# Kernel optimization log

Measured on AMD Instinct MI355X. Metric: run time of the kernel, lower is better.

Reference implementation:

```python
import jax, jax.numpy as jnp
import numpy as np

STRIDE = 16
PRE_K = 600
POST_K = 100
NMS_T = 0.7


def _gen_anchors(base=16.0, ratios=(0.5, 1.0, 2.0), scales=(8.0, 16.0, 32.0)):
    a = []
    for s in scales:
        for r in ratios:
            w = base * s * (r ** 0.5)
            h = base * s / (r ** 0.5)
            a.append([-w / 2, -h / 2, w / 2, h / 2])
    return jnp.asarray(a, jnp.float32)  # [9,4]


def _conv(x, w, b, pad):
    y = jax.lax.conv_general_dilated(x, w, (1, 1), [(pad, pad), (pad, pad)],
                                     dimension_numbers=("NCHW", "OIHW", "NCHW"))
    return y + b[None, :, None, None]


def _decode(deltas, anchors):
    w = anchors[:, 2] - anchors[:, 0]
    h = anchors[:, 3] - anchors[:, 1]
    cx = anchors[:, 0] + 0.5 * w
    cy = anchors[:, 1] + 0.5 * h
    dx, dy, dw, dh = deltas[:, 0], deltas[:, 1], deltas[:, 2], deltas[:, 3]
    pcx = cx + dx * w
    pcy = cy + dy * h
    pw = w * jnp.exp(dw)
    ph = h * jnp.exp(dh)
    return jnp.stack([pcx - 0.5 * pw, pcy - 0.5 * ph,
                      pcx + 0.5 * pw, pcy + 0.5 * ph], axis=-1)


def _nms_keep(boxes, thresh):
    # boxes already sorted by score descending; returns bool keep mask [N]
    x1, y1, x2, y2 = boxes[:, 0], boxes[:, 1], boxes[:, 2], boxes[:, 3]
    area = (x2 - x1) * (y2 - y1)
    xx1 = jnp.maximum(x1[:, None], x1[None, :])
    yy1 = jnp.maximum(y1[:, None], y1[None, :])
    xx2 = jnp.minimum(x2[:, None], x2[None, :])
    yy2 = jnp.minimum(y2[:, None], y2[None, :])
    inter = jnp.maximum(xx2 - xx1, 0.0) * jnp.maximum(yy2 - yy1, 0.0)
    iou = inter / (area[:, None] + area[None, :] - inter)
    n = boxes.shape[0]
    idx = jnp.arange(n)

    def body(i, keep):
        suppress = keep[i] & (iou[i] > thresh) & (idx > i)
        return keep & ~suppress

    return jax.lax.fori_loop(0, n, body, jnp.ones((n,), bool))


def setup_inputs() -> dict:
    key = jax.random.key(0)
    ks = jax.random.split(key, 7)
    C_in, C_mid, A = 256, 256, 9
    feats = jax.random.normal(ks[0], (4, C_in, 128, 128), jnp.float32)
    conv_w = jax.random.normal(ks[1], (C_mid, C_in, 3, 3), jnp.float32) * 0.02
    conv_b = jnp.zeros((C_mid,), jnp.float32)
    cls_w = jax.random.normal(ks[2], (A, C_mid, 1, 1), jnp.float32) * 0.05
    cls_b = jnp.zeros((A,), jnp.float32)
    bbox_w = jax.random.normal(ks[3], (A * 4, C_mid, 1, 1), jnp.float32) * 0.02
    bbox_b = jnp.zeros((A * 4,), jnp.float32)
    return {"features": feats, "conv_w": conv_w, "conv_b": conv_b,
            "cls_w": cls_w, "cls_b": cls_b, "bbox_w": bbox_w, "bbox_b": bbox_b,
            "image_h": 2048, "image_w": 2048}


def reference(features, conv_w, conv_b, cls_w, cls_b, bbox_w, bbox_b, image_h, image_w):
    B, _, H, W = features.shape
    A = cls_w.shape[0]
    t = jax.nn.relu(_conv(features, conv_w, conv_b, 1))
    logits = _conv(t, cls_w, cls_b, 0)        # [B,A,H,W]
    bbox_deltas = _conv(t, bbox_w, bbox_b, 0)  # [B,4A,H,W]

    anchors = _gen_anchors()
    sx = jnp.arange(W, dtype=jnp.float32) * STRIDE
    sy = jnp.arange(H, dtype=jnp.float32) * STRIDE
    gy, gx = jnp.meshgrid(sy, sx, indexing="ij")
    shifts = jnp.stack([gx, gy, gx, gy], axis=2).reshape(-1, 4)  # [HW,4]
    anchors_all = (anchors[None, :, :] + shifts[:, None, :]).reshape(-1, 4)  # [HW*A,4]

    scores = jnp.transpose(logits, (0, 2, 3, 1)).reshape(B, -1)          # [B,HWA]
    deltas = jnp.transpose(bbox_deltas, (0, 2, 3, 1)).reshape(B, -1, 4)  # [B,HWA,4]

    img_w = jnp.float32(image_w)
    img_h = jnp.float32(image_h)

    def per_image(s, d):
        p = _decode(d, anchors_all)
        p = jnp.stack([jnp.clip(p[:, 0], 0.0, img_w),
                       jnp.clip(p[:, 1], 0.0, img_h),
                       jnp.clip(p[:, 2], 0.0, img_w),
                       jnp.clip(p[:, 3], 0.0, img_h)], axis=-1)
        _, topi = jax.lax.top_k(s, PRE_K)
        p = p[topi]                                # [PRE_K,4] sorted by score
        keep = _nms_keep(p, NMS_T)
        order = jnp.argsort(jnp.where(keep, 0, 1), stable=True)  # kept first, score order
        sel = order[:POST_K]
        valid = keep[sel]
        return p[sel] * valid[:, None].astype(p.dtype)  # zero-pad suppressed slots

    return jax.vmap(per_image)(scores, deltas)  # [B,POST_K,4]
```

## Files before the change

kernel.cpp:

```cpp
#include <hip/hip_runtime.h>
#include <cstdint>
#include <cstddef>

#define BB 4
#define CIN 256
#define HH 128
#define WW 128
#define NANCH (HH*WW*9)
#define PRE_K 600
#define POST_K 100
#define NMS_T 0.7f
#define CAND_CAP 2048

typedef _Float16 f16x8 __attribute__((ext_vector_type(8)));
typedef float    f32x4 __attribute__((ext_vector_type(4)));

#define WS_SCORES 0
#define WS_DELTAS (BB*NANCH)
#define WS_WHI    (WS_DELTAS + BB*NANCH*4)
#define WS_WLO    (WS_WHI + 9*256*128)
#define WS_HIST   (WS_WLO + 9*256*128)
#define WS_CCNT   (WS_HIST + 8192)
#define WS_CAND   (WS_CCNT + 16)
#define WS_PHI    (WS_CAND + 16384)
#define WS_PLANE_F 8388608
#define WS_PLO    (WS_PHI + WS_PLANE_F)
#define WS_ZERO   (WS_PLO + WS_PLANE_F)
#define WS_TOTAL_FULL (WS_ZERO + 16)
#define WS_TOTAL_MIN  WS_PHI

__device__ inline unsigned score_key(float f) {
    unsigned u = __float_as_uint(f);
    return (u & 0x80000000u) ? ~u : (u | 0x80000000u);
}

__global__ __launch_bounds__(256)
void prep_all(const float* __restrict__ feat, const float* __restrict__ convw,
              _Float16* __restrict__ pHi, _Float16* __restrict__ pLo,
              _Float16* __restrict__ whi, _Float16* __restrict__ wlo,
              float* __restrict__ zeroPg, unsigned* __restrict__ ghist,
              int prepBlocks)
{
    const int blk = blockIdx.x;
    if (blk < prepBlocks) {
        const int id = blk * 256 + threadIdx.x;
        if (blk == 0 && threadIdx.x < 16) zeroPg[threadIdx.x] = 0.f;
        const int gx = id & 127;
        const int gy = (id >> 7) & 127;
        const int ck = (id >> 14) & 7;
        const int b  = id >> 17;
        const int g  = (((gx + 1) >> 1) & 1) | (((gy + 1) & 1) << 1);
        const float* fb = feat + ((size_t)(b*256 + ck*32) << 14) + (gy << 7) + gx;
        f16x8 gh[4], gl[4];
        #pragma unroll
        for (int icg = 0; icg < 4; ++icg)
            #pragma unroll
            for (int k = 0; k < 8; ++k) {
                const float v = fb[(size_t)(icg*8 + k) << 14] * 16.f;
                const _Float16 h = (_Float16)v;
                gh[icg][k] = h;
                gl[icg][k] = (_Float16)(v - (float)h);
            }
        char* Hc = (char*)pHi + (size_t)id * 64;
        char* Lc = (char*)pLo + (size_t)id * 64;
        #pragma unroll
        for (int icg = 0; icg < 4; ++icg) {
            const int p = icg ^ g;
            *(f16x8*)(Hc + p*16) = gh[icg];
            *(f16x8*)(Lc + p*16) = gl[icg];
        }
    } else if (blk < prepBlocks + 256) {
        const int g = (blk - prepBlocks) * 256 + threadIdx.x;
        if (g >= 65536) return;
        const int oc = g >> 8, ic = g & 255;
        const int chunk = ic >> 5, icl = ic & 31;
        #pragma unroll
        for (int t = 0; t < 9; ++t) {
            const float v = convw[(size_t)g*9 + t] * 64.f;
            const _Float16 h = (_Float16)v;
            const _Float16 lo = (_Float16)(v - (float)h);
            const size_t o = (size_t)((t*8 + chunk)*256 + oc)*32 + icl;
            whi[o] = h;
            wlo[o] = lo;
        }
    } else {
        const int id = (blk - prepBlocks - 256) * 256 + threadIdx.x;
        if (id < 8208) ghist[id] = 0u;
    }
}

__global__ __launch_bounds__(512, 2)
void conv_mfma(const float* __restrict__ feat, const float* __restrict__ convb,
               const _Float16* __restrict__ whi, const _Float16* __restrict__ wlo,
               const float* __restrict__ clsw, const float* __restrict__ bboxw,
               const float* __restrict__ clsb, const float* __restrict__ bboxb,
               const _Float16* __restrict__ pHi, const _Float16* __restrict__ pLo,
               const float* __restrict__ zeroPg, unsigned* __restrict__ ghist,
               float* __restrict__ scores, float* __restrict__ deltas)
{
    __shared__ __align__(16) unsigned char smem[87040];
    float* sBias = (float*)(smem + 86016);

    const int bid = blockIdx.x;
    const int b  = bid >> 6;
    const int ty = (bid >> 3) & 7;
    const int tx = bid & 7;
    const int h0 = ty*16, c0 = tx*16;
    const int tid = threadIdx.x;
    const int w   = tid >> 6;
    const int wm  = w >> 1;
    const int wph = w & 1;
    const int l  = tid & 63;
    const int q  = l >> 4;
    const int c  = l & 15;

    const float* featb = feat + (size_t)b*CIN*HH*WW;
    const int wOff = (wm*64 + c)*32 + q*8;

    if (tid < 256) sBias[tid] = convb[tid] * 1024.f;

    int sdesc[3];
    #pragma unroll
    for (int it = 0; it < 3; ++it) {
        const int e = it*512 + tid;
        if (e < 1344) {
            const int Yl = e / 72, rem = e - Yl*72;
            const int Xl = rem >> 2, p = rem & 3;
            const int gy = h0 - 1 + Yl, gx = c0 - 1 + Xl;
            sdesc[it] = (((unsigned)gy < 128u) && ((unsigned)gx < 128u))
                        ? ((((gy << 7) + gx) << 6) + (p << 4)) : -1;
        } else sdesc[it] = -2;
    }

    auto stage = [&](int ck, int buf) {
        unsigned char* hb = smem + buf*21504;
        unsigned char* lb = smem + 43008 + buf*21504;
        if (pHi) {
            const size_t pb = ((size_t)(b*8 + ck)) << 20;
            #pragma unroll
            for (int pl = 0; pl < 2; ++pl) {
                const char* Ps = (const char*)(pl ? pLo : pHi) + pb;
                unsigned char* Pd = pl ? lb : hb;
                #pragma unroll
                for (int it = 0; it < 3; ++it) {
                    if (sdesc[it] != -2) {
                        const char* src = (sdesc[it] >= 0) ? Ps + sdesc[it]
                                                           : (const char*)zeroPg;
                        __builtin_amdgcn_global_load_lds(
                            (const __attribute__((address_space(1))) void*)src,
                            (__attribute__((address_space(3))) void*)(Pd + it*8192 + tid*16),
                            16, 0, 0);
                    }
                }
            }
        } else {
            const int ic0s = ck*32;
            for (int e = tid; e < 1296; e += 512) {
                const int icg = e / 324, s = e - icg*324;
                const int Y = s / 18, X = s - Y*18;
                const int gy = h0 - 1 + Y, gx = c0 - 1 + X;
                const int g = ((X >> 1) & 1) | ((Y & 1) << 1);
                const bool inb = ((unsigned)gy < 128u) && ((unsigned)gx < 128u);
                f16x8 hv, lv;
                #pragma unroll
                for (int k = 0; k < 8; ++k) {
                    float v = 0.f;
                    if (inb) v = featb[((size_t)(ic0s + icg*8 + k)*HH + gy)*WW + gx];
                    v *= 16.f;
                    const _Float16 h = (_Float16)v;
                    hv[k] = h;
                    lv[k] = (_Float16)(v - (float)h);
                }
                const int base = s*64 + ((icg ^ g) << 4);
                *(f16x8*)(hb + base) = hv;
                *(f16x8*)(lb + base) = lv;
            }
        }
    };

    stage(0, 0);
    __syncthreads();

    f32x4 acc[4][8];
    #pragma unroll
    for (int mf = 0; mf < 4; ++mf) {
        const f32x4 bv = *(const f32x4*)(sBias + (wm*64 + mf*16 + 4*q));
        #pragma unroll
        for (int nf = 0; nf < 8; ++nf) acc[mf][nf] = bv;
    }

    for (int chunk = 0; chunk < 8; ++chunk) {
        const int cur = chunk & 1;
        if (chunk + 1 < 8) stage(chunk + 1, cur ^ 1);
        const unsigned char* hb = smem + cur*21504;
        const unsigned char* lb = smem + 43008 + cur*21504;

        #pragma unroll 3
        for (int t = 0; t < 9; ++t) {
            const int ky = t / 3, kx = t - ky*3;
            const _Float16* pWh = whi + (size_t)(t*8 + chunk)*8192 + wOff;
            const _Float16* pWl = wlo + (size_t)(t*8 + chunk)*8192 + wOff;
            f16x8 ah[4], al[4];
            #pragma unroll
            for (int mf = 0; mf < 4; ++mf) {
                ah[mf] = *(const f16x8*)(const void*)(pWh + mf*512);
                al[mf] = *(const f16x8*)(const void*)(pWl + mf*512);
            }
            #pragma unroll
            for (int nfh = 0; nfh < 2; ++nfh) {
                f16x8 bh[4], bl[4];
                #pragma unroll
                for (int j = 0; j < 4; ++j) {
                    const int nf = nfh*4 + j;
                    const int Y = wph*8 + (nf >> 1)*2 + (c >> 3) + ky;
                    const int X = (nf & 1)*8 + (c & 7) + kx;
                    const int g = ((X >> 1) & 1) | ((Y & 1) << 1);
                    const int addr = (Y*18 + X)*64 + ((q ^ g) << 4);
                    bh[j] = *(const f16x8*)(hb + addr);
                    bl[j] = *(const f16x8*)(lb + addr);
                }
                #pragma unroll
                for (int mf = 0; mf < 4; ++mf)
                    #pragma unroll
                    for (int j = 0; j < 4; ++j) {
                        acc[mf][nfh*4+j] = __builtin_amdgcn_mfma_f32_16x16x32_f16(ah[mf], bh[j], acc[mf][nfh*4+j], 0, 0, 0);
                        acc[mf][nfh*4+j] = __builtin_amdgcn_mfma_f32_16x16x32_f16(ah[mf], bl[j], acc[mf][nfh*4+j], 0, 0, 0);
                        acc[mf][nfh*4+j] = __builtin_amdgcn_mfma_f32_16x16x32_f16(al[mf], bh[j], acc[mf][nfh*4+j], 0, 0, 0);
                    }
            }
        }
        __syncthreads();
    }

    #pragma unroll
    for (int mf = 0; mf < 4; ++mf)
        #pragma unroll
        for (int nf = 0; nf < 8; ++nf)
            #pragma unroll
            for (int r = 0; r < 4; ++r)
                acc[mf][nf][r] = fmaxf(acc[mf][nf][r], 0.f) * 0.0009765625f;

    float*    sW15  = (float*)smem;
    float*    sPart = (float*)(smem + 15360);
    unsigned* sHist = (unsigned*)(smem + 76800);

    for (int e = tid; e < 2048; e += 512) sHist[e] = 0u;

    for (int g = 0; g < 3; ++g) {
        __syncthreads();
        for (int e = tid; e < 3840; e += 512) {
            const int chl = e >> 8, o = e & 255;
            const int ch = g*15 + chl;
            sW15[e] = (ch < 9) ? clsw[ch*256 + o] : bboxw[(ch - 9)*256 + o];
        }
        __syncthreads();
        for (int chl = 0; chl < 15; ++chl) {
            f32x4 wv[4];
            #pragma unroll
            for (int mf = 0; mf < 4; ++mf)
                wv[mf] = *(const f32x4*)(sW15 + chl*256 + wm*64 + mf*16 + 4*q);
            float p[8];
            #pragma unroll
            for (int nf = 0; nf < 8; ++nf) {
                float s = 0.f;
                #pragma unroll
                for (int mf = 0; mf < 4; ++mf)
                    #pragma unroll
                    for (int r = 0; r < 4; ++r)
                        s += wv[mf][r] * acc[mf][nf][r];
                s += __shfl_xor(s, 16, 64);
                s += __shfl_xor(s, 32, 64);
                p[nf] = s;
            }
            const float v0 = (q == 0) ? p[0] : (q == 1) ? p[1] : (q == 2) ? p[2] : p[3];
            const float v1 = (q == 0) ? p[4] : (q == 1) ? p[5] : (q == 2) ? p[6] : p[7];
            sPart[(w*15 + chl)*128 + q*16 + c]      = v0;
            sPart[(w*15 + chl)*128 + 64 + q*16 + c] = v1;
        }
        __syncthreads();
        for (int e = tid; e < 3840; e += 512) {
            const int chl = e >> 8, pxg = e & 255;
            const int ph = pxg >> 7, pxl = pxg & 127;
            float s = 0.f;
            #pragma unroll
            for (int wmq = 0; wmq < 4; ++wmq)
                s += sPart[((wmq*2 + ph)*15 + chl)*128 + pxl];
            const int ch = g*15 + chl;
            s += (ch < 9) ? clsb[ch] : bboxb[ch - 9];
            const int nf = pxl >> 4, cc2 = pxl & 15;
            const int Y = ph*8 + (nf >> 1)*2 + (cc2 >> 3);
            const int X = (nf & 1)*8 + (cc2 & 7);
            const int gy = h0 + Y, gx = c0 + X;
            const int n4 = gy*WW + gx;
            if (ch < 9) {
                scores[(size_t)b*NANCH + n4*9 + ch] = s;
                atomicAdd(&sHist[score_key(s) >> 21], 1u);
            } else {
                const int cc = ch - 9;
                deltas[((size_t)b*NANCH + n4*9 + (cc >> 2))*4 + (cc & 3)] = s;
            }
        }
    }
    for (int e = tid; e < 2048; e += 512) {
        const unsigned cv = sHist[e];
        if (cv) atomicAdd(&ghist[b*2048 + e], cv);
    }
}

__device__ inline void find_thresh(const unsigned* hist, int NB, unsigned target, unsigned* shv)
{
    const int tid = threadIdx.x;
    if (tid < 64) {
        const int gsz = NB >> 5;
        unsigned gsum = 0;
        if (tid < 32)
            for (int k = 0; k < gsz; ++k)
                gsum += hist[tid*gsz + ((k + tid) & (gsz-1))];
        unsigned suf = gsum;
        #pragma unroll
        for (int d = 1; d < 32; d <<= 1) {
            const unsigned t = __shfl_down(suf, d, 64);
            if (tid + d < 32) suf += t;
        }
        const unsigned long long m = __ballot(tid < 32 && suf >= target);
        const int G = 63 - __clzll(m);
        unsigned caboveG = 0;
        { const unsigned t = __shfl(suf, G+1, 64); if (G < 31) caboveG = t; }
        unsigned h = 0;
        if (tid < gsz) h = hist[G*gsz + tid];
        unsigned wsuf = h;
        #pragma unroll
        for (int d = 1; d < 64; d <<= 1) {
            const unsigned t = __shfl_down(wsuf, d, 64);
            if (tid + d < gsz) wsuf += t;
        }
        const unsigned long long m2 = __ballot(tid < gsz && (caboveG + wsuf) >= target);
        const int L = 63 - __clzll(m2);
        if (tid == L) { shv[0] = (unsigned)(G*gsz + L); shv[1] = caboveG + wsuf - h; }
    }
}

__global__ __launch_bounds__(256)
void filter_kernel(const float* __restrict__ scores, const unsigned* __restrict__ ghist,
                   unsigned* __restrict__ ccnt, unsigned long long* __restrict__ cand)
{
    __shared__ unsigned h[2048];
    __shared__ unsigned shv[8];
    const int blk = blockIdx.x;
    const int b = blk >> 6, s = blk & 63;
    const int tid = threadIdx.x;
    const unsigned* hb = ghist + b*2048;
    for (int e = tid; e < 2048; e += 256) h[e] = hb[e];
    __syncthreads();
    find_thresh(h, 2048, PRE_K, shv);
    __syncthreads();
    const unsigned T1 = shv[0];
    const unsigned C  = shv[1] + h[T1];
    const float* si = scores + (size_t)b*NANCH + s*2304;
    if (C <= (unsigned)CAND_CAP) {
        #pragma unroll
        for (int k = 0; k < 9; ++k) {
            const int i = tid + k*256;
            const unsigned u = score_key(si[i]);
            if ((u >> 21) >= T1) {
                const unsigned p = atomicAdd(&ccnt[b], 1u);
                cand[(size_t)b*CAND_CAP + p] =
                    ((unsigned long long)(~u) << 32) | (unsigned)(s*2304 + i);
            }
        }
    } else if (s == 0 && tid == 0) {
        ccnt[b] = 0x7FFFFFFFu;
    }
}

__device__ inline unsigned long long shfl_u64(unsigned long long v, int src) {
    const int lo = __shfl((int)(v & 0xffffffffull), src, 64);
    const int hi = __shfl((int)(v >> 32), src, 64);
    return ((unsigned long long)(unsigned)hi << 32) | (unsigned)lo;
}

__global__ __launch_bounds__(1024)
void post_kernel(const float* __restrict__ scores, const float* __restrict__ deltas,
                 const unsigned* __restrict__ ccnt, const unsigned long long* __restrict__ cand,
                 const int* __restrict__ imh, const int* __restrict__ imw,
                 float* __restrict__ out)
{
    __shared__ unsigned hist[2048];
    __shared__ unsigned long long arr[1024];
    __shared__ unsigned tiebuf[1024];
    __shared__ unsigned shv[8];
    __shared__ unsigned long long arr2[CAND_CAP];
    __shared__ float bx[PRE_K][4];
    __shared__ unsigned long long mrow[PRE_K][10];
    __shared__ unsigned long long keepw[10];
    __shared__ unsigned wpfx[11];
    __shared__ int sel[POST_K];
    const int b = blockIdx.x, tid = threadIdx.x;
    const float* si = scores + (size_t)b*NANCH;

    const unsigned n = ccnt[b];
    const bool fast = (n <= (unsigned)CAND_CAP);
    if (fast) {
        for (int e = tid; e < CAND_CAP; e += 1024)
            arr2[e] = (e < (int)n) ? cand[(size_t)b*CAND_CAP + e] : ~0ull;
        for (unsigned k = 2; k <= (unsigned)CAND_CAP; k <<= 1)
            for (unsigned j = k >> 1; j > 0; j >>= 1) {
                __syncthreads();
                #pragma unroll
                for (int hh = 0; hh < 2; ++hh) {
                    const unsigned i = (unsigned)tid + hh*1024, ixj = i ^ j;
                    if (ixj > i) {
                        const unsigned long long a = arr2[i], c2 = arr2[ixj];
                        if ((a > c2) == ((i & k) == 0)) { arr2[i] = c2; arr2[ixj] = a; }
                    }
                }
            }
        __syncthreads();
    } else {
        for (int i = tid; i < 2048; i += 1024) hist[i] = 0;
        __syncthreads();
        for (int i = tid; i < NANCH; i += 1024)
            atomicAdd(&hist[score_key(si[i]) >> 21], 1u);
        __syncthreads();
        find_thresh(hist, 2048, PRE_K, shv);
        __syncthreads();
        const unsigned T1 = shv[0], gtA = shv[1];
        __syncthreads();

        for (int i = tid; i < 2048; i += 1024) hist[i] = 0;
        __syncthreads();
        for (int i = tid; i < NANCH; i += 1024) {
            const unsigned u = score_key(si[i]);
            if ((u >> 21) == T1) atomicAdd(&hist[(u >> 10) & 0x7FFu], 1u);
        }
        __syncthreads();
        find_thresh(hist, 2048, PRE_K - gtA, shv);
        __syncthreads();
        const unsigned T2 = shv[0], gtB = shv[1];
        const unsigned top22 = (T1 << 11) | T2;
        __syncthreads();

        for (int i = tid; i < 1024; i += 1024) hist[i] = 0;
        __syncthreads();
        for (int i = tid; i < NANCH; i += 1024) {
            const unsigned u = score_key(si[i]);
            if ((u >> 10) == top22) atomicAdd(&hist[u & 0x3FFu], 1u);
        }
        __syncthreads();
        find_thresh(hist, 1024, PRE_K - gtA - gtB, shv);
        if (tid == 0) { shv[4] = 0; shv[5] = 0; }
        __syncthreads();
        const unsigned u_thr = (top22 << 10) | shv[0];
        const unsigned n_greater = gtA + gtB + shv[1];
        __syncthreads();

        for (int i = tid; i < NANCH; i += 1024) {
            const unsigned u = score_key(si[i]);
            if (u > u_thr) {
                const unsigned p = atomicAdd(&shv[4], 1u);
                arr[p] = ((unsigned long long)(~u) << 32) | (unsigned)i;
            } else if (u == u_thr) {
                const unsigned p = atomicAdd(&shv[5], 1u);
                if (p < 1024u) tiebuf[p] = (unsigned)i;
            }
        }
        __syncthreads();
        const unsigned cnt_tie = (shv[5] > 1024u) ? 1024u : shv[5];
        if ((unsigned)tid >= cnt_tie) tiebuf[tid] = 0xFFFFFFFFu;

        for (unsigned k = 2; k <= 1024; k <<= 1)
            for (unsigned j = k >> 1; j > 0; j >>= 1) {
                __syncthreads();
                const unsigned i = (unsigned)tid, ixj = i ^ j;
                if (ixj > i) {
                    const unsigned a = tiebuf[i], cc = tiebuf[ixj];
                    if ((a > cc) == ((i & k) == 0)) { tiebuf[i] = cc; tiebuf[ixj] = a; }
                }
            }
        __syncthreads();
        const unsigned ties_needed = PRE_K - n_greater;
        if ((unsigned)tid < ties_needed)
            arr[n_greater + tid] = ((unsigned long long)(~u_thr) << 32) | tiebuf[tid];
        if (tid >= PRE_K) arr[tid] = ~0ull;

        for (unsigned k = 2; k <= 1024; k <<= 1)
            for (unsigned j = k >> 1; j > 0; j >>= 1) {
                __syncthreads();
                const unsigned i = (unsigned)tid, ixj = i ^ j;
                if (ixj > i) {
                    const unsigned long long a = arr[i], cc = arr[ixj];
                    if ((a > cc) == ((i & k) == 0)) { arr[i] = cc; arr[ixj] = a; }
                }
            }
        __syncthreads();
        if (tid < 1024) arr2[tid] = arr[tid];
        __syncthreads();
    }

    if (tid < PRE_K) {
        const unsigned idx = (unsigned)arr2[tid];
        const int a   = (int)(idx % 9u);
        const int n4  = (int)(idx / 9u);
        const int hh_ = n4 >> 7;
        const int ww_ = n4 & 127;
        const int si_ = a / 3, ri = a % 3;
        const double sq = (ri == 0) ? 0.70710678118654752440 : ((ri == 1) ? 1.0 : 1.41421356237309504880);
        const double sc = (si_ == 0) ? 8.0 : ((si_ == 1) ? 16.0 : 32.0);
        const float half_w = (float)(16.0 * sc * sq * 0.5);
        const float half_h = (float)(16.0 * sc / sq * 0.5);
        const float shx = 16.f * (float)ww_;
        const float shy = 16.f * (float)hh_;
        const float x1a = shx - half_w, x2a = shx + half_w;
        const float y1a = shy - half_h, y2a = shy + half_h;
        const float aw = x2a - x1a, ah = y2a - y1a;
        const float acx = x1a + 0.5f*aw, acy = y1a + 0.5f*ah;
        const float* d = deltas + ((size_t)b*NANCH + idx) * 4;
        const float dx = d[0], dy = d[1], dw = d[2], dh = d[3];
        const float pcx = acx + dx*aw;
        const float pcy = acy + dy*ah;
        const float pw  = aw * expf(dw);
        const float ph  = ah * expf(dh);
        const float fw = (float)imw[0], fh = (float)imh[0];
        bx[tid][0] = fminf(fmaxf(pcx - 0.5f*pw, 0.f), fw);
        bx[tid][1] = fminf(fmaxf(pcy - 0.5f*ph, 0.f), fh);
        bx[tid][2] = fminf(fmaxf(pcx + 0.5f*pw, 0.f), fw);
        bx[tid][3] = fminf(fmaxf(pcy + 0.5f*ph, 0.f), fh);
    }
    __syncthreads();

    for (int item = tid; item < PRE_K*10; item += 1024) {
        const int i  = item / 10;
        const int wj = item - i*10;
        unsigned long long m = 0ull;
        const int jbase = wj * 64;
        if (jbase + 63 > i) {
            const float xi1 = bx[i][0], yi1 = bx[i][1], xi2 = bx[i][2], yi2 = bx[i][3];
            const float ai = (xi2 - xi1) * (yi2 - yi1);
            for (int bit = 0; bit < 64; ++bit) {
                const int j = jbase + bit;
                if (j < PRE_K && j > i) {
                    const float xx1 = fmaxf(xi1, bx[j][0]);
                    const float yy1 = fmaxf(yi1, bx[j][1]);
                    const float xx2 = fminf(xi2, bx[j][2]);
                    const float yy2 = fminf(yi2, bx[j][3]);
                    const float inter = fmaxf(xx2 - xx1, 0.f) * fmaxf(yy2 - yy1, 0.f);
                    const float aj = (bx[j][2] - bx[j][0]) * (bx[j][3] - bx[j][1]);
                    const float iou = inter / (ai + aj - inter);
                    if (iou > NMS_T) m |= (1ull << bit);
                }
            }
        }
        mrow[i][wj] = m;
    }
    __syncthreads();

    if (tid < 64) {
        const int lane = tid;
        unsigned long long kwv;
        if (lane < 9)       kwv = ~0ull;
        else if (lane == 9) kwv = (1ull << (PRE_K - 576)) - 1;
        else                kwv = 0ull;
        for (int w = 0; w < 10; ++w) {
            const int base = w*64;
            const int nb = (w == 9) ? (PRE_K - 576) : 64;
            if (lane == w) {
                for (int bit = 0; bit < nb; ++bit) {
                    const unsigned long long mm = mrow[base + bit][w];
                    if ((kwv >> bit) & 1ull) kwv &= ~mm;
                }
            }
            const unsigned long long fw = shfl_u64(kwv, w);
            if (lane > w && lane < 10) {
                for (int bit = 0; bit < nb; ++bit) {
                    const unsigned long long mm = mrow[base + bit][lane];
                    if ((fw >> bit) & 1ull) kwv &= ~mm;
                }
            }
        }
        if (lane < 10) keepw[lane] = kwv;
    }
    __syncthreads();
    if (tid == 0) {
        unsigned ccount = 0;
        #pragma unroll
        for (int w = 0; w < 10; ++w) { wpfx[w] = ccount; ccount += (unsigned)__popcll(keepw[w]); }
        wpfx[10] = ccount;
    }
    if (tid < POST_K) sel[tid] = -1;
    __syncthreads();
    if (tid < PRE_K) {
        const int w = tid >> 6, bit = tid & 63;
        const unsigned long long kw = keepw[w];
        if ((kw >> bit) & 1ull) {
            const unsigned rank = wpfx[w] + (unsigned)__popcll(kw & ((1ull << bit) - 1ull));
            if (rank < POST_K) sel[rank] = tid;
        }
    }
    __syncthreads();
    if (tid < POST_K) {
        const int s_ = sel[tid];
        float o0 = 0.f, o1 = 0.f, o2 = 0.f, o3 = 0.f;
        if (s_ >= 0) { o0 = bx[s_][0]; o1 = bx[s_][1]; o2 = bx[s_][2]; o3 = bx[s_][3]; }
        float* o = out + (size_t)b*POST_K*4 + tid*4;
        o[0] = o0; o[1] = o1; o[2] = o2; o[3] = o3;
    }
}

extern "C" void kernel_launch(void* const* d_in, const int* in_sizes, int n_in,
                              void* d_out, int out_size, void* d_ws, size_t ws_size,
                              hipStream_t stream) {
    const float* feat  = (const float*)d_in[0];
    const float* convw = (const float*)d_in[1];
    const float* convb = (const float*)d_in[2];
    const float* clsw  = (const float*)d_in[3];
    const float* clsb  = (const float*)d_in[4];
    const float* bboxw = (const float*)d_in[5];
    const float* bboxb = (const float*)d_in[6];
    const int*   imh   = (const int*)d_in[7];
    const int*   imw   = (const int*)d_in[8];

    if (ws_size < (size_t)WS_TOTAL_MIN * sizeof(float)) return;
    const bool use_prep = ws_size >= (size_t)WS_TOTAL_FULL * sizeof(float);

    float*    scores = (float*)d_ws + WS_SCORES;
    float*    deltas = (float*)d_ws + WS_DELTAS;
    _Float16* whi    = (_Float16*)((float*)d_ws + WS_WHI);
    _Float16* wlo    = (_Float16*)((float*)d_ws + WS_WLO);
    unsigned* ghist  = (unsigned*)((float*)d_ws + WS_HIST);
    unsigned* ccnt   = (unsigned*)((float*)d_ws + WS_CCNT);
    unsigned long long* cand = (unsigned long long*)((float*)d_ws + WS_CAND);
    _Float16* pHi    = use_prep ? (_Float16*)((float*)d_ws + WS_PHI) : nullptr;
    _Float16* pLo    = use_prep ? (_Float16*)((float*)d_ws + WS_PLO) : nullptr;
    float*    zeroPg = use_prep ? ((float*)d_ws + WS_ZERO) : nullptr;
    float*    outp   = (float*)d_out;

    const int prepBlocks = use_prep ? 2048 : 0;
    prep_all<<<dim3(prepBlocks + 256 + 33), dim3(256), 0, stream>>>(
        feat, convw, pHi, pLo, whi, wlo, zeroPg, ghist, prepBlocks);
    conv_mfma<<<dim3(256), dim3(512), 0, stream>>>(feat, convb, whi, wlo, clsw, bboxw,
                                                   clsb, bboxb, pHi, pLo, zeroPg, ghist,
                                                   scores, deltas);
    filter_kernel<<<dim3(256), dim3(256), 0, stream>>>(scores, ghist, ccnt, cand);
    post_kernel<<<dim3(BB), dim3(1024), 0, stream>>>(scores, deltas, ccnt, cand,
                                                     imh, imw, outp);
}
```

Baseline: 440.2 us.

## Replace candidate bitonic sort with radix-select top-K and precompute conv LDS addresses

Result: slower. 532.2 us (+20.9%).

```diff
diff --git a/kernel.cpp b/kernel.cpp
--- a/kernel.cpp
+++ b/kernel.cpp
@@ -10,7 +10,7 @@
 #define PRE_K 600
 #define POST_K 100
 #define NMS_T 0.7f
-#define CAND_CAP 2048
+#define CAND_CAP 8192
 
 typedef _Float16 f16x8 __attribute__((ext_vector_type(8)));
 typedef float    f32x4 __attribute__((ext_vector_type(4)));
@@ -22,7 +22,7 @@
 #define WS_HIST   (WS_WLO + 9*256*128)
 #define WS_CCNT   (WS_HIST + 8192)
 #define WS_CAND   (WS_CCNT + 16)
-#define WS_PHI    (WS_CAND + 16384)
+#define WS_PHI    (WS_CAND + BB*CAND_CAP*2)
 #define WS_PLANE_F 8388608
 #define WS_PLO    (WS_PHI + WS_PLANE_F)
 #define WS_ZERO   (WS_PLO + WS_PLANE_F)
@@ -118,6 +118,23 @@
     const int wOff = (wm*64 + c)*32 + q*8;
 
     if (tid < 256) sBias[tid] = convb[tid] * 1024.f;
+
+    int rcbase[8];
+    #pragma unroll
+    for (int nf = 0; nf < 8; ++nf) {
+        const int by = wph*8 + (nf >> 1)*2 + (c >> 3);
+        const int bxx = (nf & 1)*8 + (c & 7);
+        rcbase[nf] = (by*18 + bxx)*64;
+    }
+    int xort[3][2];
+    #pragma unroll
+    for (int kx = 0; kx < 3; ++kx)
+        #pragma unroll
+        for (int kyp = 0; kyp < 2; ++kyp) {
+            const int gxb = (((c & 7) + kx) >> 1) & 1;
+            const int gyb = (((c >> 3) + kyp) & 1) << 1;
+            xort[kx][kyp] = ((q ^ (gxb | gyb)) << 4);
+        }
 
     int sdesc[3];
     #pragma unroll
@@ -195,9 +212,10 @@
         const unsigned char* hb = smem + cur*21504;
         const unsigned char* lb = smem + 43008 + cur*21504;
 
-        #pragma unroll 3
+        #pragma unroll
         for (int t = 0; t < 9; ++t) {
             const int ky = t / 3, kx = t - ky*3;
+            const int tconst = (ky*18 + kx)*64;
             const _Float16* pWh = whi + (size_t)(t*8 + chunk)*8192 + wOff;
             const _Float16* pWl = wlo + (size_t)(t*8 + chunk)*8192 + wOff;
             f16x8 ah[4], al[4];
@@ -212,10 +230,7 @@
                 #pragma unroll
                 for (int j = 0; j < 4; ++j) {
                     const int nf = nfh*4 + j;
-                    const int Y = wph*8 + (nf >> 1)*2 + (c >> 3) + ky;
-                    const int X = (nf & 1)*8 + (c & 7) + kx;
-                    const int g = ((X >> 1) & 1) | ((Y & 1) << 1);
-                    const int addr = (Y*18 + X)*64 + ((q ^ g) << 4);
+                    const int addr = rcbase[nf] + tconst + xort[kx][ky & 1];
                     bh[j] = *(const f16x8*)(hb + addr);
                     bl[j] = *(const f16x8*)(lb + addr);
                 }
@@ -385,11 +400,11 @@
                  const int* __restrict__ imh, const int* __restrict__ imw,
                  float* __restrict__ out)
 {
+    __shared__ unsigned long long cnd[CAND_CAP];
     __shared__ unsigned hist[2048];
     __shared__ unsigned long long arr[1024];
     __shared__ unsigned tiebuf[1024];
     __shared__ unsigned shv[8];
-    __shared__ unsigned long long arr2[CAND_CAP];
     __shared__ float bx[PRE_K][4];
     __shared__ unsigned long long mrow[PRE_K][10];
     __shared__ unsigned long long keepw[10];
@@ -400,60 +415,84 @@
 
     const unsigned n = ccnt[b];
     const bool fast = (n <= (unsigned)CAND_CAP);
+
     if (fast) {
         for (int e = tid; e < CAND_CAP; e += 1024)
-            arr2[e] = (e < (int)n) ? cand[(size_t)b*CAND_CAP + e] : ~0ull;
-        for (unsigned k = 2; k <= (unsigned)CAND_CAP; k <<= 1)
-            for (unsigned j = k >> 1; j > 0; j >>= 1) {
-                __syncthreads();
-                #pragma unroll
-                for (int hh = 0; hh < 2; ++hh) {
-                    const unsigned i = (unsigned)tid + hh*1024, ixj = i ^ j;
-                    if (ixj > i) {
-                        const unsigned long long a = arr2[i], c2 = arr2[ixj];
-                        if ((a > c2) == ((i & k) == 0)) { arr2[i] = c2; arr2[ixj] = a; }
-                    }
-                }
-            }
-        __syncthreads();
+            cnd[e] = (e < (int)n) ? cand[(size_t)b*CAND_CAP + e] : ~0ull;
+    }
+    __syncthreads();
+
+    for (int i = tid; i < 2048; i += 1024) hist[i] = 0;
+    __syncthreads();
+    if (fast) {
+        for (int e = tid; e < (int)n; e += 1024) {
+            const unsigned u = ~(unsigned)(cnd[e] >> 32);
+            atomicAdd(&hist[u >> 21], 1u);
+        }
     } else {
-        for (int i = tid; i < 2048; i += 1024) hist[i] = 0;
-        __syncthreads();
         for (int i = tid; i < NANCH; i += 1024)
             atomicAdd(&hist[score_key(si[i]) >> 21], 1u);
-        __syncthreads();
-        find_thresh(hist, 2048, PRE_K, shv);
-        __syncthreads();
-        const unsigned T1 = shv[0], gtA = shv[1];
-        __syncthreads();
-
-        for (int i = tid; i < 2048; i += 1024) hist[i] = 0;
-        __syncthreads();
+    }
+    __syncthreads();
+    find_thresh(hist, 2048, PRE_K, shv);
+    __syncthreads();
+    const unsigned T1 = shv[0], gtA = shv[1];
+    __syncthreads();
+
+    for (int i = tid; i < 2048; i += 1024) hist[i] = 0;
+    __syncthreads();
+    if (fast) {
+        for (int e = tid; e < (int)n; e += 1024) {
+            const unsigned u = ~(unsigned)(cnd[e] >> 32);
+            if ((u >> 21) == T1) atomicAdd(&hist[(u >> 10) & 0x7FFu], 1u);
+        }
+    } else {
         for (int i = tid; i < NANCH; i += 1024) {
             const unsigned u = score_key(si[i]);
             if ((u >> 21) == T1) atomicAdd(&hist[(u >> 10) & 0x7FFu], 1u);
         }
-        __syncthreads();
-        find_thresh(hist, 2048, PRE_K - gtA, shv);
-        __syncthreads();
-        const unsigned T2 = shv[0], gtB = shv[1];
-        const unsigned top22 = (T1 << 11) | T2;
-        __syncthreads();
-
-        for (int i = tid; i < 1024; i += 1024) hist[i] = 0;
-        __syncthreads();
+    }
+    __syncthreads();
+    find_thresh(hist, 2048, PRE_K - gtA, shv);
+    __syncthreads();
+    const unsigned T2 = shv[0], gtB = shv[1];
+    const unsigned top22 = (T1 << 11) | T2;
+    __syncthreads();
+
+    for (int i = tid; i < 1024; i += 1024) hist[i] = 0;
+    __syncthreads();
+    if (fast) {
+        for (int e = tid; e < (int)n; e += 1024) {
+            const unsigned u = ~(unsigned)(cnd[e] >> 32);
+            if ((u >> 10) == top22) atomicAdd(&hist[u & 0x3FFu], 1u);
+        }
+    } else {
         for (int i = tid; i < NANCH; i += 1024) {
             const unsigned u = score_key(si[i]);
             if ((u >> 10) == top22) atomicAdd(&hist[u & 0x3FFu], 1u);
         }
-        __syncthreads();
-        find_thresh(hist, 1024, PRE_K - gtA - gtB, shv);
-        if (tid == 0) { shv[4] = 0; shv[5] = 0; }
-        __syncthreads();
-        const unsigned u_thr = (top22 << 10) | shv[0];
-        const unsigned n_greater = gtA + gtB + shv[1];
-        __syncthreads();
-
+    }
+    __syncthreads();
+    find_thresh(hist, 1024, PRE_K - gtA - gtB, shv);
+    if (tid == 0) { shv[4] = 0; shv[5] = 0; }
+    __syncthreads();
+    const unsigned u_thr = (top22 << 10) | shv[0];
+    const unsigned n_greater = gtA + gtB + shv[1];
+    __syncthreads();
+
+    if (fast) {
+        for (int e = tid; e < (int)n; e += 1024) {
+            const unsigned long long cv = cnd[e];
+            const unsigned u = ~(unsigned)(cv >> 32);
+            if (u > u_thr) {
+                const unsigned p = atomicAdd(&shv[4], 1u);
+                arr[p] = cv;
+            } else if (u == u_thr) {
+                const unsigned p = atomicAdd(&shv[5], 1u);
+                if (p < 1024u) tiebuf[p] = (unsigned)cv;
+            }
+        }
+    } else {
         for (int i = tid; i < NANCH; i += 1024) {
             const unsigned u = score_key(si[i]);
             if (u > u_thr) {
@@ -464,41 +503,39 @@
                 if (p < 1024u) tiebuf[p] = (unsigned)i;
             }
         }
-        __syncthreads();
-        const unsigned cnt_tie = (shv[5] > 1024u) ? 1024u : shv[5];
-        if ((unsigned)tid >= cnt_tie) tiebuf[tid] = 0xFFFFFFFFu;
-
-        for (unsigned k = 2; k <= 1024; k <<= 1)
-            for (unsigned j = k >> 1; j > 0; j >>= 1) {
-                __syncthreads();
-                const unsigned i = (unsigned)tid, ixj = i ^ j;
-                if (ixj > i) {
-                    const unsigned a = tiebuf[i], cc = tiebuf[ixj];
-                    if ((a > cc) == ((i & k) == 0)) { tiebuf[i] = cc; tiebuf[ixj] = a; }
-                }
-            }
-        __syncthreads();
-        const unsigned ties_needed = PRE_K - n_greater;
-        if ((unsigned)tid < ties_needed)
-            arr[n_greater + tid] = ((unsigned long long)(~u_thr) << 32) | tiebuf[tid];
-        if (tid >= PRE_K) arr[tid] = ~0ull;
-
-        for (unsigned k = 2; k <= 1024; k <<= 1)
-            for (unsigned j = k >> 1; j > 0; j >>= 1) {
-                __syncthreads();
-                const unsigned i = (unsigned)tid, ixj = i ^ j;
-                if (ixj > i) {
-                    const unsigned long long a = arr[i], cc = arr[ixj];
-                    if ((a > cc) == ((i & k) == 0)) { arr[i] = cc; arr[ixj] = a; }
-                }
-            }
-        __syncthreads();
-        if (tid < 1024) arr2[tid] = arr[tid];
-        __syncthreads();
-    }
+    }
+    __syncthreads();
+    const unsigned cnt_tie = (shv[5] > 1024u) ? 1024u : shv[5];
+    if ((unsigned)tid >= cnt_tie) tiebuf[tid] = 0xFFFFFFFFu;
+
+    for (unsigned k = 2; k <= 1024; k <<= 1)
+        for (unsigned j = k >> 1; j > 0; j >>= 1) {
+            __syncthreads();
+            const unsigned i = (unsigned)tid, ixj = i ^ j;
+            if (ixj > i) {
+                const unsigned a = tiebuf[i], cc = tiebuf[ixj];
+                if ((a > cc) == ((i & k) == 0)) { tiebuf[i] = cc; tiebuf[ixj] = a; }
+            }
+        }
+    __syncthreads();
+    const unsigned ties_needed = PRE_K - n_greater;
+    if ((unsigned)tid < ties_needed)
+        arr[n_greater + tid] = ((unsigned long long)(~u_thr) << 32) | tiebuf[tid];
+    if (tid >= PRE_K) arr[tid] = ~0ull;
+
+    for (unsigned k = 2; k <= 1024; k <<= 1)
+        for (unsigned j = k >> 1; j > 0; j >>= 1) {
+            __syncthreads();
+            const unsigned i = (unsigned)tid, ixj = i ^ j;
+            if (ixj > i) {
+                const unsigned long long a = arr[i], cc = arr[ixj];
+                if ((a > cc) == ((i & k) == 0)) { arr[i] = cc; arr[ixj] = a; }
+            }
+        }
+    __syncthreads();
 
     if (tid < PRE_K) {
-        const unsigned idx = (unsigned)arr2[tid];
+        const unsigned idx = (unsigned)arr[tid];
         const int a   = (int)(idx % 9u);
         const int n4  = (int)(idx / 9u);
         const int hh_ = n4 >> 7;
```

## Split top-k and NMS mask stages across many blocks via rank sort

Applied to the files above, without the earlier changes.

Result: faster. 395.2 us (-10.2%).

```diff
diff --git a/kernel.cpp b/kernel.cpp
--- a/kernel.cpp
+++ b/kernel.cpp
@@ -10,7 +10,7 @@
 #define PRE_K 600
 #define POST_K 100
 #define NMS_T 0.7f
-#define CAND_CAP 2048
+#define CAND_CAP 8192
 
 typedef _Float16 f16x8 __attribute__((ext_vector_type(8)));
 typedef float    f32x4 __attribute__((ext_vector_type(4)));
@@ -22,7 +22,9 @@
 #define WS_HIST   (WS_WLO + 9*256*128)
 #define WS_CCNT   (WS_HIST + 8192)
 #define WS_CAND   (WS_CCNT + 16)
-#define WS_PHI    (WS_CAND + 16384)
+#define WS_BOX6   (WS_CAND + BB*CAND_CAP*2)
+#define WS_MROW   (WS_BOX6 + BB*PRE_K*4)
+#define WS_PHI    (WS_MROW + BB*PRE_K*10*2)
 #define WS_PLANE_F 8388608
 #define WS_PLO    (WS_PHI + WS_PLANE_F)
 #define WS_ZERO   (WS_PLO + WS_PLANE_F)
@@ -32,6 +34,36 @@
 __device__ inline unsigned score_key(float f) {
     unsigned u = __float_as_uint(f);
     return (u & 0x80000000u) ? ~u : (u | 0x80000000u);
+}
+
+__device__ inline void decode_box(unsigned idx, const float* __restrict__ deltas,
+                                  int b, float fw, float fh, float* o4)
+{
+    const int a   = (int)(idx % 9u);
+    const int n4  = (int)(idx / 9u);
+    const int hh_ = n4 >> 7;
+    const int ww_ = n4 & 127;
+    const int si_ = a / 3, ri = a % 3;
+    const double sq = (ri == 0) ? 0.70710678118654752440 : ((ri == 1) ? 1.0 : 1.41421356237309504880);
+    const double sc = (si_ == 0) ? 8.0 : ((si_ == 1) ? 16.0 : 32.0);
+    const float half_w = (float)(16.0 * sc * sq * 0.5);
+    const float half_h = (float)(16.0 * sc / sq * 0.5);
+    const float shx = 16.f * (float)ww_;
+    const float shy = 16.f * (float)hh_;
+    const float x1a = shx - half_w, x2a = shx + half_w;
+    const float y1a = shy - half_h, y2a = shy + half_h;
+    const float aw = x2a - x1a, ah = y2a - y1a;
+    const float acx = x1a + 0.5f*aw, acy = y1a + 0.5f*ah;
+    const float* d = deltas + ((size_t)b*NANCH + idx) * 4;
+    const float dx = d[0], dy = d[1], dw = d[2], dh = d[3];
+    const float pcx = acx + dx*aw;
+    const float pcy = acy + dy*ah;
+    const float pw  = aw * expf(dw);
+    const float ph  = ah * expf(dh);
+    o4[0] = fminf(fmaxf(pcx - 0.5f*pw, 0.f), fw);
+    o4[1] = fminf(fmaxf(pcy - 0.5f*ph, 0.f), fh);
+    o4[2] = fminf(fmaxf(pcx + 0.5f*pw, 0.f), fw);
+    o4[3] = fminf(fmaxf(pcy + 0.5f*ph, 0.f), fh);
 }
 
 __global__ __launch_bounds__(256)
@@ -373,164 +405,53 @@
     }
 }
 
-__device__ inline unsigned long long shfl_u64(unsigned long long v, int src) {
-    const int lo = __shfl((int)(v & 0xffffffffull), src, 64);
-    const int hi = __shfl((int)(v >> 32), src, 64);
-    return ((unsigned long long)(unsigned)hi << 32) | (unsigned)lo;
-}
-
-__global__ __launch_bounds__(1024)
-void post_kernel(const float* __restrict__ scores, const float* __restrict__ deltas,
-                 const unsigned* __restrict__ ccnt, const unsigned long long* __restrict__ cand,
+__global__ __launch_bounds__(256)
+void rank_kernel(const unsigned* __restrict__ ccnt, const unsigned long long* __restrict__ cand,
+                 const float* __restrict__ deltas,
                  const int* __restrict__ imh, const int* __restrict__ imw,
-                 float* __restrict__ out)
+                 float* __restrict__ boxes6)
 {
-    __shared__ unsigned hist[2048];
-    __shared__ unsigned long long arr[1024];
-    __shared__ unsigned tiebuf[1024];
-    __shared__ unsigned shv[8];
-    __shared__ unsigned long long arr2[CAND_CAP];
+    __shared__ unsigned long long cnd[CAND_CAP];
+    const int blk = blockIdx.x;
+    const int b = blk >> 5, s = blk & 31;
+    const int tid = threadIdx.x;
+    const unsigned n = ccnt[b];
+    if (n > (unsigned)CAND_CAP) return;
+    const int e0 = s*256;
+    if ((unsigned)e0 >= n) return;
+    for (int e = tid; e < (int)n; e += 256)
+        cnd[e] = cand[(size_t)b*CAND_CAP + e];
+    __syncthreads();
+    const int e = e0 + tid;
+    if (e >= (int)n) return;
+    const unsigned long long cv = cnd[e];
+    unsigned rank = 0;
+    for (int e2 = 0; e2 < (int)n; ++e2)
+        rank += (cnd[e2] < cv) ? 1u : 0u;
+    if (rank < PRE_K) {
+        float o4[4];
+        decode_box((unsigned)cv, deltas, b, (float)imw[0], (float)imh[0], o4);
+        float* o = boxes6 + ((size_t)b*PRE_K + rank)*4;
+        o[0] = o4[0]; o[1] = o4[1]; o[2] = o4[2]; o[3] = o4[3];
+    }
+}
+
+__global__ __launch_bounds__(256)
+void nmsmask_kernel(const unsigned* __restrict__ ccnt, const float* __restrict__ boxes6,
+                    unsigned long long* __restrict__ gmrow)
+{
     __shared__ float bx[PRE_K][4];
-    __shared__ unsigned long long mrow[PRE_K][10];
-    __shared__ unsigned long long keepw[10];
-    __shared__ unsigned wpfx[11];
-    __shared__ int sel[POST_K];
-    const int b = blockIdx.x, tid = threadIdx.x;
-    const float* si = scores + (size_t)b*NANCH;
-
+    const int blk = blockIdx.x;
+    const int b = blk / 10, rg = blk - b*10;
+    const int tid = threadIdx.x;
     const unsigned n = ccnt[b];
-    const bool fast = (n <= (unsigned)CAND_CAP);
-    if (fast) {
-        for (int e = tid; e < CAND_CAP; e += 1024)
-            arr2[e] = (e < (int)n) ? cand[(size_t)b*CAND_CAP + e] : ~0ull;
-        for (unsigned k = 2; k <= (unsigned)CAND_CAP; k <<= 1)
-            for (unsigned j = k >> 1; j > 0; j >>= 1) {
-                __syncthreads();
-                #pragma unroll
-                for (int hh = 0; hh < 2; ++hh) {
-                    const unsigned i = (unsigned)tid + hh*1024, ixj = i ^ j;
-                    if (ixj > i) {
-                        const unsigned long long a = arr2[i], c2 = arr2[ixj];
-                        if ((a > c2) == ((i & k) == 0)) { arr2[i] = c2; arr2[ixj] = a; }
-                    }
-                }
-            }
-        __syncthreads();
-    } else {
-        for (int i = tid; i < 2048; i += 1024) hist[i] = 0;
-        __syncthreads();
-        for (int i = tid; i < NANCH; i += 1024)
-            atomicAdd(&hist[score_key(si[i]) >> 21], 1u);
-        __syncthreads();
-        find_thresh(hist, 2048, PRE_K, shv);
-        __syncthreads();
-        const unsigned T1 = shv[0], gtA = shv[1];
-        __syncthreads();
-
-        for (int i = tid; i < 2048; i += 1024) hist[i] = 0;
-        __syncthreads();
-        for (int i = tid; i < NANCH; i += 1024) {
-            const unsigned u = score_key(si[i]);
-            if ((u >> 21) == T1) atomicAdd(&hist[(u >> 10) & 0x7FFu], 1u);
-        }
-        __syncthreads();
-        find_thresh(hist, 2048, PRE_K - gtA, shv);
-        __syncthreads();
-        const unsigned T2 = shv[0], gtB = shv[1];
-        const unsigned top22 = (T1 << 11) | T2;
-        __syncthreads();
-
-        for (int i = tid; i < 1024; i += 1024) hist[i] = 0;
-        __syncthreads();
-        for (int i = tid; i < NANCH; i += 1024) {
-            const unsigned u = score_key(si[i]);
-            if ((u >> 10) == top22) atomicAdd(&hist[u & 0x3FFu], 1u);
-        }
-        __syncthreads();
-        find_thresh(hist, 1024, PRE_K - gtA - gtB, shv);
-        if (tid == 0) { shv[4] = 0; shv[5] = 0; }
-        __syncthreads();
-        const unsigned u_thr = (top22 << 10) | shv[0];
-        const unsigned n_greater = gtA + gtB + shv[1];
-        __syncthreads();
-
-        for (int i = tid; i < NANCH; i += 1024) {
-            const unsigned u = score_key(si[i]);
-            if (u > u_thr) {
-                const unsigned p = atomicAdd(&shv[4], 1u);
-                arr[p] = ((unsigned long long)(~u) << 32) | (unsigned)i;
-            } else if (u == u_thr) {
-                const unsigned p = atomicAdd(&shv[5], 1u);
-                if (p < 1024u) tiebuf[p] = (unsigned)i;
-            }
-        }
-        __syncthreads();
-        const unsigned cnt_tie = (shv[5] > 1024u) ? 1024u : shv[5];
-        if ((unsigned)tid >= cnt_tie) tiebuf[tid] = 0xFFFFFFFFu;
-
-        for (unsigned k = 2; k <= 1024; k <<= 1)
-            for (unsigned j = k >> 1; j > 0; j >>= 1) {
-                __syncthreads();
-                const unsigned i = (unsigned)tid, ixj = i ^ j;
-                if (ixj > i) {
-                    const unsigned a = tiebuf[i], cc = tiebuf[ixj];
-                    if ((a > cc) == ((i & k) == 0)) { tiebuf[i] = cc; tiebuf[ixj] = a; }
-                }
-            }
-        __syncthreads();
-        const unsigned ties_needed = PRE_K - n_greater;
-        if ((unsigned)tid < ties_needed)
-            arr[n_greater + tid] = ((unsigned long long)(~u_thr) << 32) | tiebuf[tid];
-        if (tid >= PRE_K) arr[tid] = ~0ull;
-
-        for (unsigned k = 2; k <= 1024; k <<= 1)
-            for (unsigned j = k >> 1; j > 0; j >>= 1) {
-                __syncthreads();
-                const unsigned i = (unsigned)tid, ixj = i ^ j;
-                if (ixj > i) {
-                    const unsigned long long a = arr[i], cc = arr[ixj];
-                    if ((a > cc) == ((i & k) == 0)) { arr[i] = cc; arr[ixj] = a; }
-                }
-            }
-        __syncthreads();
-        if (tid < 1024) arr2[tid] = arr[tid];
-        __syncthreads();
-    }
-
-    if (tid < PRE_K) {
-        const unsigned idx = (unsigned)arr2[tid];
-        const int a   = (int)(idx % 9u);
-        const int n4  = (int)(idx / 9u);
-        const int hh_ = n4 >> 7;
-        const int ww_ = n4 & 127;
-        const int si_ = a / 3, ri = a % 3;
-        const double sq = (ri == 0) ? 0.70710678118654752440 : ((ri == 1) ? 1.0 : 1.41421356237309504880);
-        const double sc = (si_ == 0) ? 8.0 : ((si_ == 1) ? 16.0 : 32.0);
-        const float half_w = (float)(16.0 * sc * sq * 0.5);
-        const float half_h = (float)(16.0 * sc / sq * 0.5);
-        const float shx = 16.f * (float)ww_;
-        const float shy = 16.f * (float)hh_;
-        const float x1a = shx - half_w, x2a = shx + half_w;
-        const float y1a = shy - half_h, y2a = shy + half_h;
-        const float aw = x2a - x1a, ah = y2a - y1a;
-        const float acx = x1a + 0.5f*aw, acy = y1a + 0.5f*ah;
-        const float* d = deltas + ((size_t)b*NANCH + idx) * 4;
-        const float dx = d[0], dy = d[1], dw = d[2], dh = d[3];
-        const float pcx = acx + dx*aw;
-        const float pcy = acy + dy*ah;
-        const float pw  = aw * expf(dw);
-        const float ph  = ah * expf(dh);
-        const float fw = (float)imw[0], fh = (float)imh[0];
-        bx[tid][0] = fminf(fmaxf(pcx - 0.5f*pw, 0.f), fw);
-        bx[tid][1] = fminf(fmaxf(pcy - 0.5f*ph, 0.f), fh);
-        bx[tid][2] = fminf(fmaxf(pcx + 0.5f*pw, 0.f), fw);
-        bx[tid][3] = fminf(fmaxf(pcy + 0.5f*ph, 0.f), fh);
-    }
+    if (n > (unsigned)CAND_CAP) return;
+    for (int e = tid; e < PRE_K*4; e += 256)
+        bx[e >> 2][e & 3] = boxes6[(size_t)b*PRE_K*4 + e];
     __syncthreads();
-
-    for (int item = tid; item < PRE_K*10; item += 1024) {
-        const int i  = item / 10;
-        const int wj = item - i*10;
+    for (int item = tid; item < 600; item += 256) {
+        const int i  = rg*60 + item/10;
+        const int wj = item - (item/10)*10;
         unsigned long long m = 0ull;
         const int jbase = wj * 64;
         if (jbase + 63 > i) {
@@ -550,9 +471,155 @@
                 }
             }
         }
-        mrow[i][wj] = m;
-    }
-    __syncthreads();
+        gmrow[((size_t)b*PRE_K + i)*10 + wj] = m;
+    }
+}
+
+__device__ inline unsigned long long shfl_u64(unsigned long long v, int src) {
+    const int lo = __shfl((int)(v & 0xffffffffull), src, 64);
+    const int hi = __shfl((int)(v >> 32), src, 64);
+    return ((unsigned long long)(unsigned)hi << 32) | (unsigned)lo;
+}
+
+__global__ __launch_bounds__(1024)
+void post_kernel(const float* __restrict__ scores, const float* __restrict__ deltas,
+                 const unsigned* __restrict__ ccnt,
+                 const float* __restrict__ boxes6, const unsigned long long* __restrict__ gmrow,
+                 const int* __restrict__ imh, const int* __restrict__ imw,
+                 float* __restrict__ out)
+{
+    __shared__ unsigned hist[2048];
+    __shared__ unsigned long long arr[1024];
+    __shared__ unsigned tiebuf[1024];
+    __shared__ unsigned shv[8];
+    __shared__ float bx[PRE_K][4];
+    __shared__ unsigned long long mrow[PRE_K][10];
+    __shared__ unsigned long long keepw[10];
+    __shared__ unsigned wpfx[11];
+    __shared__ int sel[POST_K];
+    const int b = blockIdx.x, tid = threadIdx.x;
+    const float* si = scores + (size_t)b*NANCH;
+
+    const unsigned n = ccnt[b];
+    const bool fast = (n <= (unsigned)CAND_CAP);
+
+    if (fast) {
+        for (int e = tid; e < PRE_K*4; e += 1024)
+            bx[e >> 2][e & 3] = boxes6[(size_t)b*PRE_K*4 + e];
+        for (int e = tid; e < PRE_K*10; e += 1024)
+            mrow[e/10][e - (e/10)*10] = gmrow[(size_t)b*PRE_K*10 + e];
+        __syncthreads();
+    } else {
+        for (int i = tid; i < 2048; i += 1024) hist[i] = 0;
+        __syncthreads();
+        for (int i = tid; i < NANCH; i += 1024)
+            atomicAdd(&hist[score_key(si[i]) >> 21], 1u);
+        __syncthreads();
+        find_thresh(hist, 2048, PRE_K, shv);
+        __syncthreads();
+        const unsigned T1 = shv[0], gtA = shv[1];
+        __syncthreads();
+
+        for (int i = tid; i < 2048; i += 1024) hist[i] = 0;
+        __syncthreads();
+        for (int i = tid; i < NANCH; i += 1024) {
+            const unsigned u = score_key(si[i]);
+            if ((u >> 21) == T1) atomicAdd(&hist[(u >> 10) & 0x7FFu], 1u);
+        }
+        __syncthreads();
+        find_thresh(hist, 2048, PRE_K - gtA, shv);
+        __syncthreads();
+        const unsigned T2 = shv[0], gtB = shv[1];
+        const unsigned top22 = (T1 << 11) | T2;
+        __syncthreads();
+
+        for (int i = tid; i < 1024; i += 1024) hist[i] = 0;
+        __syncthreads();
+        for (int i = tid; i < NANCH; i += 1024) {
+            const unsigned u = score_key(si[i]);
+            if ((u >> 10) == top22) atomicAdd(&hist[u & 0x3FFu], 1u);
+        }
+        __syncthreads();
+        find_thresh(hist, 1024, PRE_K - gtA - gtB, shv);
+        if (tid == 0) { shv[4] = 0; shv[5] = 0; }
+        __syncthreads();
+        const unsigned u_thr = (top22 << 10) | shv[0];
+        const unsigned n_greater = gtA + gtB + shv[1];
+        __syncthreads();
+
+        for (int i = tid; i < NANCH; i += 1024) {
+            const unsigned u = score_key(si[i]);
+            if (u > u_thr) {
+                const unsigned p = atomicAdd(&shv[4], 1u);
+                arr[p] = ((unsigned long long)(~u) << 32) | (unsigned)i;
+            } else if (u == u_thr) {
+                const unsigned p = atomicAdd(&shv[5], 1u);
+                if (p < 1024u) tiebuf[p] = (unsigned)i;
+            }
+        }
+        __syncthreads();
+        const unsigned cnt_tie = (shv[5] > 1024u) ? 1024u : shv[5];
+        if ((unsigned)tid >= cnt_tie) tiebuf[tid] = 0xFFFFFFFFu;
+
+        for (unsigned k = 2; k <= 1024; k <<= 1)
+            for (unsigned j = k >> 1; j > 0; j >>= 1) {
+                __syncthreads();
+                const unsigned i = (unsigned)tid, ixj = i ^ j;
+                if (ixj > i) {
+                    const unsigned a = tiebuf[i], cc = tiebuf[ixj];
+                    if ((a > cc) == ((i & k) == 0)) { tiebuf[i] = cc; tiebuf[ixj] = a; }
+                }
+            }
+        __syncthreads();
+        const unsigned ties_needed = PRE_K - n_greater;
+        if ((unsigned)tid < ties_needed)
+            arr[n_greater + tid] = ((unsigned long long)(~u_thr) << 32) | tiebuf[tid];
+        if (tid >= PRE_K) arr[tid] = ~0ull;
+
+        for (unsigned k = 2; k <= 1024; k <<= 1)
+            for (unsigned j = k >> 1; j > 0; j >>= 1) {
+                __syncthreads();
+                const unsigned i = (unsigned)tid, ixj = i ^ j;
+                if (ixj > i) {
+                    const unsigned long long a = arr[i], cc = arr[ixj];
+                    if ((a > cc) == ((i & k) == 0)) { arr[i] = cc; arr[ixj] = a; }
+                }
+            }
+        __syncthreads();
+
+        if (tid < PRE_K) {
+            float o4[4];
+            decode_box((unsigned)arr[tid], deltas, b, (float)imw[0], (float)imh[0], o4);
+            bx[tid][0] = o4[0]; bx[tid][1] = o4[1]; bx[tid][2] = o4[2]; bx[tid][3] = o4[3];
+        }
+        __syncthreads();
+
+        for (int item = tid; item < PRE_K*10; item += 1024) {
+            const int i  = item / 10;
+            const int wj = item - i*10;
+            unsigned long long m = 0ull;
+            const int jbase = wj * 64;
+            if (jbase + 63 > i) {
+                const float xi1 = bx[i][0], yi1 = bx[i][1], xi2 = bx[i][2], yi2 = bx[i][3];
+                const float ai = (xi2 - xi1) * (yi2 - yi1);
+                for (int bit = 0; bit < 64; ++bit) {
+                    const int j = jbase + bit;
+                    if (j < PRE_K && j > i) {
+                        const float xx1 = fmaxf(xi1, bx[j][0]);
+                        const float yy1 = fmaxf(yi1, bx[j][1]);
+                        const float xx2 = fminf(xi2, bx[j][2]);
+                        const float yy2 = fminf(yi2, bx[j][3]);
+                        const float inter = fmaxf(xx2 - xx1, 0.f) * fmaxf(yy2 - yy1, 0.f);
+                        const float aj = (bx[j][2] - bx[j][0]) * (bx[j][3] - bx[j][1]);
+                        const float iou = inter / (ai + aj - inter);
+                        if (iou > NMS_T) m |= (1ull << bit);
+                    }
+                }
+            }
+            mrow[i][wj] = m;
+        }
+        __syncthreads();
+    }
 
     if (tid < 64) {
         const int lane = tid;
@@ -629,6 +696,8 @@
     unsigned* ghist  = (unsigned*)((float*)d_ws + WS_HIST);
     unsigned* ccnt   = (unsigned*)((float*)d_ws + WS_CCNT);
     unsigned long long* cand = (unsigned long long*)((float*)d_ws + WS_CAND);
+    float*    boxes6 = (float*)d_ws + WS_BOX6;
+    unsigned long long* gmrow = (unsigned long long*)((float*)d_ws + WS_MROW);
     _Float16* pHi    = use_prep ? (_Float16*)((float*)d_ws + WS_PHI) : nullptr;
     _Float16* pLo    = use_prep ? (_Float16*)((float*)d_ws + WS_PLO) : nullptr;
     float*    zeroPg = use_prep ? ((float*)d_ws + WS_ZERO) : nullptr;
@@ -641,6 +710,8 @@
                                                    clsb, bboxb, pHi, pLo, zeroPg, ghist,
                                                    scores, deltas);
     filter_kernel<<<dim3(256), dim3(256), 0, stream>>>(scores, ghist, ccnt, cand);
-    post_kernel<<<dim3(BB), dim3(1024), 0, stream>>>(scores, deltas, ccnt, cand,
+    rank_kernel<<<dim3(128), dim3(256), 0, stream>>>(ccnt, cand, deltas, imh, imw, boxes6);
+    nmsmask_kernel<<<dim3(40), dim3(256), 0, stream>>>(ccnt, boxes6, gmrow);
+    post_kernel<<<dim3(BB), dim3(1024), 0, stream>>>(scores, deltas, ccnt, boxes6, gmrow,
                                                      imh, imw, outp);
 }
```
